# Performance work log

Measured on AMD Instinct MI355X. Metric: run time of the kernel, lower is better.

The kernel has to match this reference:

```python
import jax, jax.numpy as jnp
import numpy as np

N = 20000      # number of boxes / graph nodes
E = 160000     # random edges (before self-loops)
DIM = 1024     # feature dim (SIA default)


def setup_inputs() -> dict:
    key = jax.random.key(0)
    ks = jax.random.split(key, 12)
    feats = jax.random.normal(ks[0], (N, DIM), dtype=jnp.float32)
    boxes = jax.random.uniform(ks[1], (N, 4), dtype=jnp.float32)
    src = jax.random.randint(ks[2], (E,), 0, N, dtype=jnp.int32)
    dst = jax.random.randint(ks[3], (E,), 0, N, dtype=jnp.int32)
    loop = jnp.arange(N, dtype=jnp.int32)
    # dgl.add_self_loop: every node gets a self edge
    edges_src = jnp.concatenate([src, loop])
    edges_dst = jnp.concatenate([dst, loop])
    s = 0.02
    return {
        'feats': feats, 'boxes': boxes,
        'edges_src': edges_src, 'edges_dst': edges_dst,
        'w_pos1': jax.random.normal(ks[4], (4, DIM), jnp.float32) * s,
        'b_pos1': jnp.zeros((DIM,), jnp.float32),
        'w_pos2': jax.random.normal(ks[5], (DIM, DIM), jnp.float32) * s,
        'b_pos2': jnp.zeros((DIM,), jnp.float32),
        'w_g1': jax.random.normal(ks[6], (DIM, DIM), jnp.float32) * s,
        'b_g1': jnp.zeros((DIM,), jnp.float32),
        'w_g2': jax.random.normal(ks[7], (DIM, DIM), jnp.float32) * s,
        'b_g2': jnp.zeros((DIM,), jnp.float32),
    }


def _graph_conv(h, src, dst, w, b, n):
    # DGL GraphConv, norm='both', in_feats == out_feats => aggregate then matmul.
    ones = jnp.ones(src.shape, dtype=h.dtype)
    out_deg = jax.ops.segment_sum(ones, src, num_segments=n)
    in_deg = jax.ops.segment_sum(ones, dst, num_segments=n)
    norm_src = jnp.where(out_deg > 0, jax.lax.rsqrt(jnp.maximum(out_deg, 1.0)), 0.0)
    norm_dst = jnp.where(in_deg > 0, jax.lax.rsqrt(jnp.maximum(in_deg, 1.0)), 0.0)
    h = h * norm_src[:, None]
    agg = jax.ops.segment_sum(h[src], dst, num_segments=n)  # irregular gather/scatter
    agg = agg * norm_dst[:, None]
    return agg @ w + b


def reference(feats, boxes, edges_src, edges_dst,
              w_pos1, b_pos1, w_pos2, b_pos2,
              w_g1, b_g1, w_g2, b_g2):
    n = feats.shape[0]
    boxes = jnp.clip(boxes, -10.0, 10.0)
    pos = jax.nn.relu(boxes @ w_pos1 + b_pos1) @ w_pos2 + b_pos2
    h = feats + pos
    h = _graph_conv(h, edges_src, edges_dst, w_g1, b_g1, n)
    h = jax.nn.relu(h)  # dropout is identity in eval
    h = _graph_conv(h, edges_src, edges_dst, w_g2, b_g2, n)
    return h.mean(0)  # frame token [DIM]
```

## Files before the change

kernel.cpp:

```cpp
#include <hip/hip_runtime.h>
#include <hip/hip_bf16.h>
#include <stdint.h>

#define DIM 1024

typedef __attribute__((ext_vector_type(4))) float f32x4;
typedef __attribute__((ext_vector_type(2))) float f32x2;
typedef __attribute__((ext_vector_type(8))) short short8;

__device__ __forceinline__ float bf2f(ushort u) {
    union { uint32_t u; float f; } c; c.u = ((uint32_t)u) << 16; return c.f;
}
__device__ __forceinline__ ushort f2bf(float f) {
    union { float f; uint32_t u; } c; c.f = f;
    uint32_t r = (c.u + 0x7fffu + ((c.u >> 16) & 1u)) >> 16;
    return (ushort)r;
}
__device__ __forceinline__ uint8_t f2fp8(float v) {
    int b;
    asm("v_cvt_pk_fp8_f32 %0, %1, %2" : "=v"(b) : "v"(v), "v"(v));
    return (uint8_t)b;
}
__device__ __forceinline__ void acc_fp8x4(uint32_t dw, float* a) {
    f32x2 lo, hi;
    asm("v_cvt_pk_f32_fp8 %0, %1" : "=v"(lo) : "v"(dw));
    uint32_t dwh = dw >> 16;
    asm("v_cvt_pk_f32_fp8 %0, %1" : "=v"(hi) : "v"(dwh));
    a[0] += lo[0]; a[1] += lo[1]; a[2] += hi[0]; a[3] += hi[1];
}

__device__ __forceinline__ void async_copy16(void* lds, const void* g) {
    __builtin_amdgcn_global_load_lds((const __attribute__((address_space(1))) void*)g,
                                     (__attribute__((address_space(3))) void*)lds, 16, 0, 0);
}


__global__ void deg_kernel(const int* __restrict__ src, const int* __restrict__ dst,
                           int* out_deg, int* in_deg, int ee) {
    int e = blockIdx.x * 256 + threadIdx.x;
    if (e < ee) {
        atomicAdd(&out_deg[src[e]], 1);
        atomicAdd(&in_deg[dst[e]], 1);
    }
}

__global__ void norm_kernel(const int* __restrict__ out_deg, const int* __restrict__ in_deg,
                            float* ns, float* nd, int n) {
    int i = blockIdx.x * 256 + threadIdx.x;
    if (i < n) {
        int od = out_deg[i], id = in_deg[i];
        ns[i] = od > 0 ? rsqrtf((float)od) : 0.f;
        nd[i] = id > 0 ? rsqrtf((float)id) : 0.f;
    }
}

__global__ void csum_kernel(const int* __restrict__ src, const int* __restrict__ dst,
                            const float* __restrict__ nd, float* cw, int ee) {
    int e = blockIdx.x * 256 + threadIdx.x;
    if (e < ee) atomicAdd(&cw[src[e]], nd[dst[e]]);
}

__global__ void scan_kernel(const int* __restrict__ deg, int* row_ptr, int* cursor, int n) {
    __shared__ int wsum[16];
    __shared__ int carry_s;
    int tid = threadIdx.x, lane = tid & 63, wid = tid >> 6;
    if (tid == 0) carry_s = 0;
    __syncthreads();
    for (int base = 0; base < n; base += 1024) {
        int x = (base + tid < n) ? deg[base + tid] : 0;
        int v = x;
#pragma unroll
        for (int off = 1; off < 64; off <<= 1) {
            int u = __shfl_up(v, off);
            if (lane >= off) v += u;
        }
        if (lane == 63) wsum[wid] = v;
        __syncthreads();
        if (wid == 0 && lane < 16) {
            int wv = wsum[lane];
#pragma unroll
            for (int off = 1; off < 16; off <<= 1) {
                int wu = __shfl_up(wv, off);
                if (lane >= off) wv += wu;
            }
            wsum[lane] = wv;
        }
        __syncthreads();
        int waveoff = (wid > 0) ? wsum[wid - 1] : 0;
        if (base + tid < n) {
            int ex = carry_s + waveoff + v - x;
            row_ptr[base + tid] = ex;
            cursor[base + tid] = ex;
        }
        __syncthreads();
        if (tid == 0) carry_s += wsum[15];
        __syncthreads();
    }
}

__global__ void wnode_kernel(float* cw, const float* __restrict__ ns, int n) {
    int i = blockIdx.x * 256 + threadIdx.x;
    if (i < n) cw[i] *= ns[i];
}

__global__ void scatter_kernel(const int* __restrict__ src, const int* __restrict__ dst,
                               int* cursor, int* csr_src, int ee) {
    int e = blockIdx.x * 256 + threadIdx.x;
    if (e < ee) {
        int p = atomicAdd(&cursor[dst[e]], 1);
        csr_src[p] = src[e];
    }
}


__global__ __launch_bounds__(256) void posA_kernel(const float* __restrict__ boxes,
                                                   const float* __restrict__ w1,
                                                   const float* __restrict__ b1,
                                                   ushort* __restrict__ t, int n) {
    int lane = threadIdx.x & 63, wid = threadIdx.x >> 6;
    int wave = blockIdx.x * 4 + wid, nw = gridDim.x * 4;
    int c0 = lane * 16;
    for (int row = wave; row < n; row += nw) {
        float b[4];
#pragma unroll
        for (int j = 0; j < 4; j++) {
            float v = boxes[row * 4 + j];
            b[j] = fminf(fmaxf(v, -10.f), 10.f);
        }
        short8 o[2];
#pragma unroll
        for (int h = 0; h < 2; h++) {
#pragma unroll
            for (int q = 0; q < 8; q++) {
                int col = c0 + h * 8 + q;
                float v = b1[col];
#pragma unroll
                for (int j = 0; j < 4; j++) v = fmaf(b[j], w1[j * DIM + col], v);
                o[h][q] = (short)f2bf(fmaxf(v, 0.f));
            }
        }
        *(short8*)(t + (size_t)row * DIM + c0) = o[0];
        *(short8*)(t + (size_t)row * DIM + c0 + 8) = o[1];
    }
}


__global__ __launch_bounds__(256) void transpose_bf16_kernel(const float* __restrict__ w,
                                                             ushort* __restrict__ wt) {
    __shared__ float tile[32][33];
    int bx = blockIdx.x, by = blockIdx.y;
    int tx = threadIdx.x & 31, ty = threadIdx.x >> 5;
#pragma unroll
    for (int r = 0; r < 32; r += 8)
        tile[ty + r][tx] = w[(size_t)(by * 32 + ty + r) * DIM + bx * 32 + tx];
    __syncthreads();
#pragma unroll
    for (int r = 0; r < 32; r += 8)
        wt[(size_t)(bx * 32 + ty + r) * DIM + by * 32 + tx] = f2bf(tile[tx][ty + r]);
}


template <int EPI>
__global__ __launch_bounds__(512, 4) void gemm_kernel(
    const ushort* __restrict__ A, const ushort* __restrict__ Bt,
    const float* __restrict__ bias, const float* __restrict__ feats,
    const float* __restrict__ nsrc, void* __restrict__ outp,
    int mtiles, int mreal) {
    __shared__ __align__(128) ushort ldsA[2][128 * 64];
    __shared__ __align__(128) ushort ldsB[2][128 * 64];
    int j = blockIdx.x;
    int xcd = j & 7, kq = j >> 3;
    int bm = xcd + 8 * (kq >> 3);
    int bn = kq & 7;
    if (bm >= mtiles) return;

    int tid = threadIdx.x, lane = tid & 63, wid = tid >> 6;
    int wm = wid >> 1, wn = wid & 1;

    f32x4 acc[2][4];
#pragma unroll
    for (int m = 0; m < 2; m++)
#pragma unroll
        for (int nn = 0; nn < 4; nn++) acc[m][nn] = (f32x4){0.f, 0.f, 0.f, 0.f};

    int srow = wid * 8 + (lane >> 3);
    int sseg = (lane & 7) ^ (lane >> 3);
    const ushort* gA = A + (size_t)(bm * 128 + srow) * DIM + sseg * 8;
    const ushort* gB = Bt + (size_t)(bn * 128 + srow) * DIM + sseg * 8;
    int ldsoff0 = (wid * 8) * 64;

    int r16 = lane & 15, khi = lane >> 4;

    auto stage = [&](int buf, int kt) {
#pragma unroll
        for (int c = 0; c < 2; c++) {
            async_copy16(&ldsA[buf][ldsoff0 + c * 64 * 64], gA + (size_t)c * 64 * DIM + kt * 64);
            async_copy16(&ldsB[buf][ldsoff0 + c * 64 * 64], gB + (size_t)c * 64 * DIM + kt * 64);
        }
    };

    stage(0, 0);
    int cur = 0;
    for (int kt = 0; kt < DIM / 64; ++kt) {
        if (kt + 1 < DIM / 64) {
            stage(cur ^ 1, kt + 1);
            asm volatile("s_waitcnt vmcnt(4)" ::: "memory");
        } else {
            asm volatile("s_waitcnt vmcnt(0)" ::: "memory");
        }
        __builtin_amdgcn_s_barrier();
        __builtin_amdgcn_sched_barrier(0);
#pragma unroll
        for (int kk = 0; kk < 2; kk++) {
            short8 af[2], bfv[4];
#pragma unroll
            for (int m = 0; m < 2; m++) {
                int row = wm * 32 + m * 16 + r16;
                int seg = (kk * 4 + khi) ^ (row & 7);
                af[m] = *(const short8*)&ldsA[cur][row * 64 + seg * 8];
            }
#pragma unroll
            for (int nn = 0; nn < 4; nn++) {
                int row = wn * 64 + nn * 16 + r16;
                int seg = (kk * 4 + khi) ^ (row & 7);
                bfv[nn] = *(const short8*)&ldsB[cur][row * 64 + seg * 8];
            }
#pragma unroll
            for (int m = 0; m < 2; m++)
#pragma unroll
                for (int nn = 0; nn < 4; nn++)
                    acc[m][nn] = __builtin_amdgcn_mfma_f32_16x16x32_bf16(af[m], bfv[nn], acc[m][nn], 0, 0, 0);
        }
        __builtin_amdgcn_sched_barrier(0);
        __builtin_amdgcn_s_barrier();
        cur ^= 1;
    }

    int colbase = bn * 128 + wn * 64;
    int rowbase = bm * 128 + wm * 32 + khi * 4;
    if (EPI == 1) {
        ushort* ob = (ushort*)outp;
#pragma unroll
        for (int m = 0; m < 2; m++) {
#pragma unroll
            for (int jj = 0; jj < 4; jj++) {
                int r = rowbase + m * 16 + jj;
                if (r < mreal) {
                    float ns = nsrc[r];
#pragma unroll
                    for (int nn = 0; nn < 4; nn++) {
                        int col = colbase + nn * 16 + r16;
                        float v = acc[m][nn][jj] + bias[col] + feats[(size_t)r * DIM + col];
                        ob[(size_t)r * DIM + col] = f2bf(v * ns);
                    }
                }
            }
        }
    } else {
        uint8_t* o8 = (uint8_t*)outp;
#pragma unroll
        for (int m = 0; m < 2; m++) {
#pragma unroll
            for (int jj = 0; jj < 4; jj++) {
                int r = rowbase + m * 16 + jj;
                if (r < mreal) {
#pragma unroll
                    for (int nn = 0; nn < 4; nn++) {
                        int col = colbase + nn * 16 + r16;
                        o8[(size_t)r * DIM + col] = f2fp8(acc[m][nn][jj] * 16.f);
                    }
                }
            }
        }
    }
}


__global__ __launch_bounds__(256) void agg2_kernel(
    const uint8_t* __restrict__ z8, const int* __restrict__ row_ptr,
    const int* __restrict__ in_deg, const int* __restrict__ csr_src,
    const float* __restrict__ ndst, const float* __restrict__ wnode,
    const float* __restrict__ bg1, float* __restrict__ vec, int n) {
    __shared__ float red[DIM];
    int lane = threadIdx.x & 63, wid = threadIdx.x >> 6;
    int wave = blockIdx.x * 4 + wid;
    int nwaves = gridDim.x * 4;
    int c0 = lane * 16;

    float bv[16];
#pragma unroll
    for (int t = 0; t < 16; t++) bv[t] = bg1[c0 + t];
    float part[16];
#pragma unroll
    for (int t = 0; t < 16; t++) part[t] = 0.f;

    for (int node = wave; node < n; node += nwaves) {
        int start = row_ptr[node], cnt = in_deg[node];
        float a[16];
#pragma unroll
        for (int t = 0; t < 16; t++) a[t] = 0.f;
        int e = 0;
        for (; e + 8 <= cnt; e += 8) {
            uint4 v[8];
#pragma unroll
            for (int q = 0; q < 8; q++)
                v[q] = *(const uint4*)(z8 + (size_t)csr_src[start + e + q] * DIM + c0);
#pragma unroll
            for (int q = 0; q < 8; q++) {
                acc_fp8x4(v[q].x, a + 0);
                acc_fp8x4(v[q].y, a + 4);
                acc_fp8x4(v[q].z, a + 8);
                acc_fp8x4(v[q].w, a + 12);
            }
        }
        for (; e < cnt; e++) {
            uint4 v0 = *(const uint4*)(z8 + (size_t)csr_src[start + e] * DIM + c0);
            acc_fp8x4(v0.x, a + 0);
            acc_fp8x4(v0.y, a + 4);
            acc_fp8x4(v0.z, a + 8);
            acc_fp8x4(v0.w, a + 12);
        }
        float nd16 = ndst[node] * 0.0625f, w = wnode[node];
#pragma unroll
        for (int t = 0; t < 16; t++)
            part[t] = fmaf(w, fmaxf(fmaf(nd16, a[t], bv[t]), 0.f), part[t]);
    }

    if (wid == 0) {
#pragma unroll
        for (int t = 0; t < 16; t++) red[c0 + t] = part[t];
    }
    __syncthreads();
    for (int w = 1; w < 4; ++w) {
        if (wid == w) {
#pragma unroll
            for (int t = 0; t < 16; t++) red[c0 + t] += part[t];
        }
        __syncthreads();
    }
    for (int c = threadIdx.x; c < DIM; c += 256) atomicAdd(&vec[c], red[c]);
}


__global__ __launch_bounds__(256) void final_kernel(const float* __restrict__ vec,
                                                    const float* __restrict__ w2,
                                                    const float* __restrict__ b2,
                                                    float* out, float invn) {
    int d = blockIdx.x * 256 + threadIdx.x;
    int kb = blockIdx.y * 128;
    float acc = 0.f;
#pragma unroll 4
    for (int k = 0; k < 128; k++) acc = fmaf(vec[kb + k], w2[(size_t)(kb + k) * DIM + d], acc);
    float add = acc * invn + (blockIdx.y == 0 ? b2[d] : 0.f);
    atomicAdd(&out[d], add);
}


extern "C" void kernel_launch(void* const* d_in, const int* in_sizes, int n_in,
                              void* d_out, int out_size, void* d_ws, size_t ws_size,
                              hipStream_t stream) {
    const float* feats  = (const float*)d_in[0];
    const float* boxes  = (const float*)d_in[1];
    const int*   esrc   = (const int*)d_in[2];
    const int*   edst   = (const int*)d_in[3];
    const float* w_pos1 = (const float*)d_in[4];
    const float* b_pos1 = (const float*)d_in[5];
    const float* w_pos2 = (const float*)d_in[6];
    const float* b_pos2 = (const float*)d_in[7];
    const float* w_g1   = (const float*)d_in[8];
    const float* b_g1   = (const float*)d_in[9];
    const float* w_g2   = (const float*)d_in[10];
    const float* b_g2   = (const float*)d_in[11];

    int n = in_sizes[0] / DIM;
    int ee = in_sizes[2];
    int mtiles = (n + 127) / 128;
    int groups = (mtiles + 7) / 8;
    int gemm_grid = groups * 64;

    char* p = (char*)d_ws;
    auto alloc = [&](size_t bytes) -> char* {
        char* r = p;
        p += (bytes + 255) & ~((size_t)255);
        return r;
    };
    size_t mp = (size_t)mtiles * 128;
    ushort* t_z    = (ushort*)alloc(mp * DIM * 2);
    ushort* hs     = (ushort*)alloc(mp * DIM * 2);
    ushort* wt1    = (ushort*)alloc((size_t)DIM * DIM * 2);
    ushort* wt2    = (ushort*)alloc((size_t)DIM * DIM * 2);
    char* zero_base = p;
    int*   out_deg = (int*)alloc((size_t)n * 4);
    int*   in_deg  = (int*)alloc((size_t)n * 4);
    float* cw      = (float*)alloc((size_t)n * 4);
    float* vec     = (float*)alloc((size_t)DIM * 4);
    size_t zero_bytes = (size_t)(p - zero_base);
    float* nsrc    = (float*)alloc((size_t)n * 4);
    float* ndst    = (float*)alloc((size_t)n * 4);
    int*   row_ptr = (int*)alloc((size_t)(n + 1) * 4);
    int*   cursor  = (int*)alloc((size_t)n * 4);
    int*   csr_src = (int*)alloc((size_t)ee * 4);

    hipMemsetAsync(zero_base, 0, zero_bytes, stream);
    hipMemsetAsync(d_out, 0, (size_t)out_size * 4, stream);

    int eb = (ee + 255) / 256;
    int nb = (n + 255) / 256;

    deg_kernel<<<eb, 256, 0, stream>>>(esrc, edst, out_deg, in_deg, ee);
    posA_kernel<<<256, 256, 0, stream>>>(boxes, w_pos1, b_pos1, t_z, n);
    transpose_bf16_kernel<<<dim3(32, 32), 256, 0, stream>>>(w_pos2, wt1);
    transpose_bf16_kernel<<<dim3(32, 32), 256, 0, stream>>>(w_g1, wt2);
    norm_kernel<<<nb, 256, 0, stream>>>(out_deg, in_deg, nsrc, ndst, n);
    csum_kernel<<<eb, 256, 0, stream>>>(esrc, edst, ndst, cw, ee);
    scan_kernel<<<1, 1024, 0, stream>>>(in_deg, row_ptr, cursor, n);
    wnode_kernel<<<nb, 256, 0, stream>>>(cw, nsrc, n);
    scatter_kernel<<<eb, 256, 0, stream>>>(esrc, edst, cursor, csr_src, ee);

    gemm_kernel<1><<<gemm_grid, 512, 0, stream>>>(t_z, wt1, b_pos2, feats, nsrc, (void*)hs,
                                                  mtiles, n);
    uint8_t* z8 = (uint8_t*)t_z;
    gemm_kernel<0><<<gemm_grid, 512, 0, stream>>>(hs, wt2, nullptr, nullptr, nullptr, (void*)z8,
                                                  mtiles, n);
    agg2_kernel<<<2048, 256, 0, stream>>>(z8, row_ptr, in_deg, csr_src, ndst, cw, b_g1, vec, n);
    final_kernel<<<dim3(4, 8), 256, 0, stream>>>(vec, w_g2, b_g2, (float*)d_out, 1.0f / (float)n);
}
```

Baseline: 424.2 us.

## Fuse preprocessing kernels and memsets to cut launch count

Merges the two weight transposes, the box-position MLP and the zeroing memsets into one block-partitioned prep kernel. Degree normalization moves into the scan kernel, and the column-sum and CSR scatter become a single edge kernel. The per-node ns multiply moves into agg2. This removes about eight launches and two memset calls of fixed overhead, at the cost of a heterogeneous kernel whose branches run unevenly.

Measured after the change: 419.3 us. Within noise of the previous version (-1.2%).

```diff
diff --git a/kernel.cpp b/kernel.cpp
--- a/kernel.cpp
+++ b/kernel.cpp
@@ -35,6 +35,70 @@
 }
 
 
+__device__ void transpose_tile(const float* __restrict__ w, ushort* __restrict__ wt,
+                               int bx, int by, int tid) {
+    __shared__ float tile[32][33];
+    int tx = tid & 31, ty = tid >> 5;
+#pragma unroll
+    for (int r = 0; r < 32; r += 8)
+        tile[ty + r][tx] = w[(size_t)(by * 32 + ty + r) * DIM + bx * 32 + tx];
+    __syncthreads();
+#pragma unroll
+    for (int r = 0; r < 32; r += 8)
+        wt[(size_t)(bx * 32 + ty + r) * DIM + by * 32 + tx] = f2bf(tile[tx][ty + r]);
+}
+
+__global__ __launch_bounds__(256) void prep_kernel(
+    const float* __restrict__ w_pos2, ushort* __restrict__ wt1,
+    const float* __restrict__ w_g1, ushort* __restrict__ wt2,
+    const float* __restrict__ boxes, const float* __restrict__ w1,
+    const float* __restrict__ b1, ushort* __restrict__ t, int n,
+    float* __restrict__ zero_base, int zero_words,
+    float* __restrict__ d_out, int out_words) {
+    int bid = blockIdx.x, tid = threadIdx.x;
+    if (bid < 1024) {
+        transpose_tile(w_pos2, wt1, bid & 31, bid >> 5, tid);
+    } else if (bid < 2048) {
+        int b = bid - 1024;
+        transpose_tile(w_g1, wt2, b & 31, b >> 5, tid);
+    } else if (bid < 2304) {
+        int pb = bid - 2048;
+        int lane = tid & 63, wid = tid >> 6;
+        int wave = pb * 4 + wid, nw = 1024;
+        int c0 = lane * 16;
+        for (int row = wave; row < n; row += nw) {
+            float b[4];
+#pragma unroll
+            for (int j = 0; j < 4; j++) {
+                float v = boxes[row * 4 + j];
+                b[j] = fminf(fmaxf(v, -10.f), 10.f);
+            }
+            short8 o[2];
+#pragma unroll
+            for (int h = 0; h < 2; h++) {
+#pragma unroll
+                for (int q = 0; q < 8; q++) {
+                    int col = c0 + h * 8 + q;
+                    float v = b1[col];
+#pragma unroll
+                    for (int j = 0; j < 4; j++) v = fmaf(b[j], w1[j * DIM + col], v);
+                    o[h][q] = (short)f2bf(fmaxf(v, 0.f));
+                }
+            }
+            *(short8*)(t + (size_t)row * DIM + c0) = o[0];
+            *(short8*)(t + (size_t)row * DIM + c0 + 8) = o[1];
+        }
+    } else {
+        int zb = bid - 2304;
+        int i = (zb * 256 + tid) * 4;
+        int stride = 8 * 256 * 4;
+        for (; i + 3 < zero_words; i += stride)
+            *(f32x4*)(zero_base + i) = (f32x4){0.f, 0.f, 0.f, 0.f};
+        for (int d = zb * 256 + tid; d < out_words; d += 8 * 256) d_out[d] = 0.f;
+    }
+}
+
+
 __global__ void deg_kernel(const int* __restrict__ src, const int* __restrict__ dst,
                            int* out_deg, int* in_deg, int ee) {
     int e = blockIdx.x * 256 + threadIdx.x;
@@ -44,30 +108,16 @@
     }
 }
 
-__global__ void norm_kernel(const int* __restrict__ out_deg, const int* __restrict__ in_deg,
-                            float* ns, float* nd, int n) {
-    int i = blockIdx.x * 256 + threadIdx.x;
-    if (i < n) {
-        int od = out_deg[i], id = in_deg[i];
-        ns[i] = od > 0 ? rsqrtf((float)od) : 0.f;
-        nd[i] = id > 0 ? rsqrtf((float)id) : 0.f;
-    }
-}
-
-__global__ void csum_kernel(const int* __restrict__ src, const int* __restrict__ dst,
-                            const float* __restrict__ nd, float* cw, int ee) {
-    int e = blockIdx.x * 256 + threadIdx.x;
-    if (e < ee) atomicAdd(&cw[src[e]], nd[dst[e]]);
-}
-
-__global__ void scan_kernel(const int* __restrict__ deg, int* row_ptr, int* cursor, int n) {
+
+__global__ void scan_kernel(const int* __restrict__ in_deg, const int* __restrict__ out_deg,
+                            int* row_ptr, int* cursor, float* ns, float* nd, int n) {
     __shared__ int wsum[16];
     __shared__ int carry_s;
     int tid = threadIdx.x, lane = tid & 63, wid = tid >> 6;
     if (tid == 0) carry_s = 0;
     __syncthreads();
     for (int base = 0; base < n; base += 1024) {
-        int x = (base + tid < n) ? deg[base + tid] : 0;
+        int x = (base + tid < n) ? in_deg[base + tid] : 0;
         int v = x;
 #pragma unroll
         for (int off = 1; off < 64; off <<= 1) {
@@ -88,9 +138,13 @@
         __syncthreads();
         int waveoff = (wid > 0) ? wsum[wid - 1] : 0;
         if (base + tid < n) {
+            int i = base + tid;
             int ex = carry_s + waveoff + v - x;
-            row_ptr[base + tid] = ex;
-            cursor[base + tid] = ex;
+            row_ptr[i] = ex;
+            cursor[i] = ex;
+            int od = out_deg[i];
+            ns[i] = od > 0 ? rsqrtf((float)od) : 0.f;
+            nd[i] = x > 0 ? rsqrtf((float)x) : 0.f;
         }
         __syncthreads();
         if (tid == 0) carry_s += wsum[15];
@@ -98,65 +152,17 @@
     }
 }
 
-__global__ void wnode_kernel(float* cw, const float* __restrict__ ns, int n) {
-    int i = blockIdx.x * 256 + threadIdx.x;
-    if (i < n) cw[i] *= ns[i];
-}
-
-__global__ void scatter_kernel(const int* __restrict__ src, const int* __restrict__ dst,
-                               int* cursor, int* csr_src, int ee) {
+
+__global__ void edge_kernel(const int* __restrict__ src, const int* __restrict__ dst,
+                            const float* __restrict__ nd, float* cw,
+                            int* cursor, int* csr_src, int ee) {
     int e = blockIdx.x * 256 + threadIdx.x;
     if (e < ee) {
-        int p = atomicAdd(&cursor[dst[e]], 1);
-        csr_src[p] = src[e];
-    }
-}
-
-
-__global__ __launch_bounds__(256) void posA_kernel(const float* __restrict__ boxes,
-                                                   const float* __restrict__ w1,
-                                                   const float* __restrict__ b1,
-                                                   ushort* __restrict__ t, int n) {
-    int lane = threadIdx.x & 63, wid = threadIdx.x >> 6;
-    int wave = blockIdx.x * 4 + wid, nw = gridDim.x * 4;
-    int c0 = lane * 16;
-    for (int row = wave; row < n; row += nw) {
-        float b[4];
-#pragma unroll
-        for (int j = 0; j < 4; j++) {
-            float v = boxes[row * 4 + j];
-            b[j] = fminf(fmaxf(v, -10.f), 10.f);
-        }
-        short8 o[2];
-#pragma unroll
-        for (int h = 0; h < 2; h++) {
-#pragma unroll
-            for (int q = 0; q < 8; q++) {
-                int col = c0 + h * 8 + q;
-                float v = b1[col];
-#pragma unroll
-                for (int j = 0; j < 4; j++) v = fmaf(b[j], w1[j * DIM + col], v);
-                o[h][q] = (short)f2bf(fmaxf(v, 0.f));
-            }
-        }
-        *(short8*)(t + (size_t)row * DIM + c0) = o[0];
-        *(short8*)(t + (size_t)row * DIM + c0 + 8) = o[1];
-    }
-}
-
-
-__global__ __launch_bounds__(256) void transpose_bf16_kernel(const float* __restrict__ w,
-                                                             ushort* __restrict__ wt) {
-    __shared__ float tile[32][33];
-    int bx = blockIdx.x, by = blockIdx.y;
-    int tx = threadIdx.x & 31, ty = threadIdx.x >> 5;
-#pragma unroll
-    for (int r = 0; r < 32; r += 8)
-        tile[ty + r][tx] = w[(size_t)(by * 32 + ty + r) * DIM + bx * 32 + tx];
-    __syncthreads();
-#pragma unroll
-    for (int r = 0; r < 32; r += 8)
-        wt[(size_t)(bx * 32 + ty + r) * DIM + by * 32 + tx] = f2bf(tile[tx][ty + r]);
+        int s = src[e], d = dst[e];
+        atomicAdd(&cw[s], nd[d]);
+        int p = atomicAdd(&cursor[d], 1);
+        csr_src[p] = s;
+    }
 }
 
 
@@ -279,8 +285,9 @@
 __global__ __launch_bounds__(256) void agg2_kernel(
     const uint8_t* __restrict__ z8, const int* __restrict__ row_ptr,
     const int* __restrict__ in_deg, const int* __restrict__ csr_src,
-    const float* __restrict__ ndst, const float* __restrict__ wnode,
-    const float* __restrict__ bg1, float* __restrict__ vec, int n) {
+    const float* __restrict__ ndst, const float* __restrict__ cw,
+    const float* __restrict__ ns, const float* __restrict__ bg1,
+    float* __restrict__ vec, int n) {
     __shared__ float red[DIM];
     int lane = threadIdx.x & 63, wid = threadIdx.x >> 6;
     int wave = blockIdx.x * 4 + wid;
@@ -320,7 +327,8 @@
             acc_fp8x4(v0.z, a + 8);
             acc_fp8x4(v0.w, a + 12);
         }
-        float nd16 = ndst[node] * 0.0625f, w = wnode[node];
+        float nd16 = ndst[node] * 0.0625f;
+        float w = cw[node] * ns[node];
 #pragma unroll
         for (int t = 0; t < 16; t++)
             part[t] = fmaf(w, fmaxf(fmaf(nd16, a[t], bv[t]), 0.f), part[t]);
@@ -401,27 +409,20 @@
     int*   cursor  = (int*)alloc((size_t)n * 4);
     int*   csr_src = (int*)alloc((size_t)ee * 4);
 
-    hipMemsetAsync(zero_base, 0, zero_bytes, stream);
-    hipMemsetAsync(d_out, 0, (size_t)out_size * 4, stream);
-
     int eb = (ee + 255) / 256;
-    int nb = (n + 255) / 256;
-
+
+    prep_kernel<<<2312, 256, 0, stream>>>(w_pos2, wt1, w_g1, wt2, boxes, w_pos1, b_pos1,
+                                          t_z, n, (float*)zero_base, (int)(zero_bytes / 4),
+                                          (float*)d_out, out_size);
     deg_kernel<<<eb, 256, 0, stream>>>(esrc, edst, out_deg, in_deg, ee);
-    posA_kernel<<<256, 256, 0, stream>>>(boxes, w_pos1, b_pos1, t_z, n);
-    transpose_bf16_kernel<<<dim3(32, 32), 256, 0, stream>>>(w_pos2, wt1);
-    transpose_bf16_kernel<<<dim3(32, 32), 256, 0, stream>>>(w_g1, wt2);
-    norm_kernel<<<nb, 256, 0, stream>>>(out_deg, in_deg, nsrc, ndst, n);
-    csum_kernel<<<eb, 256, 0, stream>>>(esrc, edst, ndst, cw, ee);
-    scan_kernel<<<1, 1024, 0, stream>>>(in_deg, row_ptr, cursor, n);
-    wnode_kernel<<<nb, 256, 0, stream>>>(cw, nsrc, n);
-    scatter_kernel<<<eb, 256, 0, stream>>>(esrc, edst, cursor, csr_src, ee);
-
+    scan_kernel<<<1, 1024, 0, stream>>>(in_deg, out_deg, row_ptr, cursor, nsrc, ndst, n);
+    edge_kernel<<<eb, 256, 0, stream>>>(esrc, edst, ndst, cw, cursor, csr_src, ee);
     gemm_kernel<1><<<gemm_grid, 512, 0, stream>>>(t_z, wt1, b_pos2, feats, nsrc, (void*)hs,
                                                   mtiles, n);
     uint8_t* z8 = (uint8_t*)t_z;
     gemm_kernel<0><<<gemm_grid, 512, 0, stream>>>(hs, wt2, nullptr, nullptr, nullptr, (void*)z8,
                                                   mtiles, n);
-    agg2_kernel<<<2048, 256, 0, stream>>>(z8, row_ptr, in_deg, csr_src, ndst, cw, b_g1, vec, n);
+    agg2_kernel<<<2048, 256, 0, stream>>>(z8, row_ptr, in_deg, csr_src, ndst, cw, nsrc,
+                                          b_g1, vec, n);
     final_kernel<<<dim3(4, 8), 256, 0, stream>>>(vec, w_g2, b_g2, (float*)d_out, 1.0f / (float)n);
 }
```
